# Kernel tuning notes

Hardware: AMD Instinct MI355X
Metric: run time of the kernel (lower is better)

## Reference

```python
import jax, jax.numpy as jnp
import numpy as np

N = 50000      # nodes
E = 1600000    # edges (avg degree 32)
IN = 4         # in_size
H = 64         # hidden size


def _gcn_conv(x, W, b, src, dst, ew, n):
    """PyG GCNConv with edge_weight: add self-loops (weight 1), symmetric
    deg^{-1/2} normalization, gather-transform-scatter aggregation, then bias."""
    xw = x @ W  # [n, out] transform first (PyG lin before propagate)
    loops = jnp.arange(n)
    s = jnp.concatenate([src, loops])
    d = jnp.concatenate([dst, loops])
    w = jnp.concatenate([ew, jnp.ones((n,), ew.dtype)])
    deg = jax.ops.segment_sum(w, d, num_segments=n)
    dinv = jnp.where(deg > 0, jax.lax.rsqrt(deg), 0.0)
    norm = dinv[s] * w * dinv[d]                      # [E+n]
    msg = xw[s] * norm[:, None]                       # [E+n, out]
    out = jax.ops.segment_sum(msg, d, num_segments=n)
    return out + b


def _tower(x, src, dst, ew, W0, b0, W1, b1, W2, b2, Wl, bl):
    # basic_gcn: GCNConv+ReLU, GCNConv+ReLU, GCNConv, then nn.Linear(out,out)
    n = x.shape[0]
    h = jax.nn.relu(_gcn_conv(x, W0, b0, src, dst, ew, n))
    h = jax.nn.relu(_gcn_conv(h, W1, b1, src, dst, ew, n))
    h = _gcn_conv(h, W2, b2, src, dst, ew, n)
    return h @ Wl + bl


def setup_inputs() -> dict:
    key = jax.random.key(0)
    ks = jax.random.split(key, 20)
    x = jax.random.normal(ks[0], (N, IN), dtype=jnp.float32)
    edge_index = jax.random.randint(ks[1], (2, E), 0, N, dtype=jnp.int64)
    edge_weights = jax.random.uniform(ks[2], (E,), dtype=jnp.float32)

    def lin(k, fin, fout):
        return jax.random.normal(k, (fin, fout), dtype=jnp.float32) * (1.0 / np.sqrt(fin))

    inp = {"x": x, "edge_index": edge_index, "edge_weights": edge_weights}
    # optim tower: in_size=4 -> 64 -> 64 -> 1, plus Linear(1,1)
    inp["o_W0"], inp["o_b0"] = lin(ks[3], IN, H), jnp.zeros((H,), jnp.float32)
    inp["o_W1"], inp["o_b1"] = lin(ks[4], H, H), jnp.zeros((H,), jnp.float32)
    inp["o_W2"], inp["o_b2"] = lin(ks[5], H, 1), jnp.zeros((1,), jnp.float32)
    inp["o_Wl"], inp["o_bl"] = lin(ks[6], 1, 1), jnp.zeros((1,), jnp.float32)
    # gamma tower: in_size+1=5 -> 64 -> 64 -> 1, plus Linear(1,1)
    inp["g_W0"], inp["g_b0"] = lin(ks[7], IN + 1, H), jnp.zeros((H,), jnp.float32)
    inp["g_W1"], inp["g_b1"] = lin(ks[8], H, H), jnp.zeros((H,), jnp.float32)
    inp["g_W2"], inp["g_b2"] = lin(ks[9], H, 1), jnp.zeros((1,), jnp.float32)
    inp["g_Wl"], inp["g_bl"] = lin(ks[10], 1, 1), jnp.zeros((1,), jnp.float32)
    return inp


def reference(x, edge_index, edge_weights,
              o_W0, o_b0, o_W1, o_b1, o_W2, o_b2, o_Wl, o_bl,
              g_W0, g_b0, g_W1, g_b1, g_W2, g_b2, g_Wl, g_bl):
    src, dst = edge_index[0], edge_index[1]
    # x_sol = optim tower (constraints=None -> no range scaling)
    x_sol = _tower(x, src, dst, edge_weights,
                   o_W0, o_b0, o_W1, o_b1, o_W2, o_b2, o_Wl, o_bl)  # [N,1]
    # gamma tower on cat(x, x_sol[:, -1:]); constraints=[0,1] -> sigmoid scaling
    xin = jnp.concatenate([x, x_sol[:, -1:]], axis=1)               # [N,5]
    g = _tower(xin, src, dst, edge_weights,
               g_W0, g_b0, g_W1, g_b1, g_W2, g_b2, g_Wl, g_bl)      # [N,1]
    gamma = jax.nn.sigmoid(g)  # scale_to_range(x, [0,1])
    # s == g == 1: gated residual combine
    x_new = x[:, -1:] + gamma * (x_sol - x[:, -1:])
    return (x_new, gamma)
```

## Files before the change

kernel.cpp:

```cpp
#include <hip/hip_runtime.h>
#include <hip/hip_fp16.h>
#include <math.h>

#define NN 50000
#define NE 1600000
#define NBK 196
#define EPB 4096
#define CAP 9216

typedef unsigned int u32;
typedef _Float16 f16x8 __attribute__((ext_vector_type(8)));
typedef float f32x4 __attribute__((ext_vector_type(4)));

static inline int cdiv(int a, int b){ return (a + b - 1) / b; }



__global__ void k_bucket(const int* __restrict__ src, const int* __restrict__ dst,
                         const float* __restrict__ ew, int* __restrict__ bcur,
                         int2* __restrict__ seL, int e){
  __shared__ int h[NBK], base[NBK], curL[NBK];
  int t = threadIdx.x;
  for (int b = t; b < NBK; b += 256){ h[b] = 0; curL[b] = 0; }
  __syncthreads();
  int beg = blockIdx.x*EPB;
  int d[16];
  #pragma unroll
  for (int i = 0; i < 16; ++i){
    int idx = beg + t + i*256;
    d[i] = (idx < e) ? dst[idx] : -1;
    if (d[i] >= 0) atomicAdd(&h[d[i] >> 8], 1);
  }
  __syncthreads();
  for (int b = t; b < NBK; b += 256)
    if (h[b] > 0) base[b] = b*CAP + atomicAdd(&bcur[b], h[b]);
  __syncthreads();
  #pragma unroll
  for (int i = 0; i < 16; ++i){
    int idx = beg + t + i*256;
    if (idx >= e) continue;
    int dd = d[i], b = dd >> 8;
    int pos = base[b] + atomicAdd(&curL[b], 1);
    seL[pos] = make_int2(((dd & 255) << 16) | src[idx], __float_as_int(ew[idx]));
  }
}

__global__ void k_csr_bucket(const int* __restrict__ bcur, const int2* __restrict__ seL,
                             const float* __restrict__ x, int* __restrict__ rowS,
                             int* __restrict__ rowE, u32* __restrict__ packed,
                             float* __restrict__ dinv, float* __restrict__ xd, int n){
  __shared__ int hist[256], sh[256], cur[256];
  __shared__ float wsum[256];
  int b = blockIdx.x, t = threadIdx.x;
  int ebeg = b*CAP, eend = ebeg + bcur[b];
  hist[t] = 0; wsum[t] = 0.f;
  __syncthreads();
  for (int i = ebeg + t; i < eend; i += 256)
    atomicAdd(&hist[seL[i].x >> 16], 1);
  __syncthreads();
  int v = hist[t];
  sh[t] = v; __syncthreads();
  for (int o = 1; o < 256; o <<= 1){
    int u = (t >= o) ? sh[t-o] : 0;
    __syncthreads();
    sh[t] += u;
    __syncthreads();
  }
  int rs = ebeg + sh[t] - v;
  int node = b*256 + t;
  if (node < n){ rowS[node] = rs; rowE[node] = rs + v; }
  cur[t] = rs;
  __syncthreads();
  for (int i = ebeg + t; i < eend; i += 256){
    int2 u = seL[i];
    int d = u.x >> 16;
    int pos = atomicAdd(&cur[d], 1);
    float w = __int_as_float(u.y);
    packed[pos] = (u32)(u.x & 0xFFFF) |
                  ((u32)__half_as_ushort(__float2half(w)) << 16);
    atomicAdd(&wsum[d], w);
  }
  __syncthreads();
  if (node < n){
    float di = rsqrtf(1.f + wsum[t]);
    dinv[node] = di;
    float4 xv = ((const float4*)x)[node];
    ((float4*)xd)[node] = make_float4(xv.x*di, xv.y*di, xv.z*di, xv.w*di);
  }
}


__global__ void k_agg4(const int* __restrict__ rowS, const int* __restrict__ rowE,
                       const u32* __restrict__ packed, const float* __restrict__ xd,
                       const float* __restrict__ dinv, float* __restrict__ y4, int n){
  int i = blockIdx.x*256 + threadIdx.x;
  if (i >= n) return;
  float4 self = ((const float4*)xd)[i];
  float ax = self.x, ay = self.y, az = self.z, aw = self.w;
  int end = rowE[i];
  for (int p = rowS[i]; p < end; ++p){
    u32 v = packed[p];
    float w = __half2float(__ushort_as_half((unsigned short)(v >> 16)));
    float4 xs = ((const float4*)xd)[v & 0xFFFF];
    ax = fmaf(w, xs.x, ax);
    ay = fmaf(w, xs.y, ay);
    az = fmaf(w, xs.z, az);
    aw = fmaf(w, xs.w, aw);
  }
  float di = dinv[i];
  ((float4*)y4)[i] = make_float4(ax*di, ay*di, az*di, aw*di);
}

template<int FIN>
__global__ __attribute__((amdgpu_waves_per_eu(2, 4)))
void k_conv2_mfma(const float* __restrict__ y4, const float* __restrict__ yx,
                  const float* __restrict__ W0, const float* __restrict__ b0,
                  const float* __restrict__ W1, const float* __restrict__ dinv,
                  __half* __restrict__ out, int n){
  int lane = threadIdx.x & 63;
  int m = lane & 15, q = lane >> 4;
  int wid = (blockIdx.x*256 + threadIdx.x) >> 6;
  int nw = gridDim.x * 4;

  auto ldB = [&](int kk, int ct){
    f16x8 r;
    #pragma unroll
    for (int j = 0; j < 8; ++j)
      r[j] = (_Float16)W1[(kk*32 + q*8 + j)*64 + ct*16 + m];
    return r;
  };
  f16x8 b00 = ldB(0,0), b01 = ldB(0,1), b02 = ldB(0,2), b03 = ldB(0,3);
  f16x8 b10 = ldB(1,0), b11 = ldB(1,1), b12 = ldB(1,2), b13 = ldB(1,3);

  float w0c[2][FIN][8];
  float b0c[2][8];
  #pragma unroll
  for (int kk = 0; kk < 2; ++kk){
    #pragma unroll
    for (int j = 0; j < 8; ++j) b0c[kk][j] = b0[kk*32 + q*8 + j];
    #pragma unroll
    for (int c = 0; c < FIN; ++c)
      #pragma unroll
      for (int j = 0; j < 8; ++j)
        w0c[kk][c][j] = W0[c*64 + kk*32 + q*8 + j];
  }

  int ntiles = n >> 4;
  for (int tile = wid; tile < ntiles; tile += nw){
    int base = tile << 4;
    float4 yv = ((const float4*)y4)[base + m];
    float y5 = 0.f;
    if constexpr (FIN == 5) y5 = yx[base + m];
    f16x8 a0, a1;
    #pragma unroll
    for (int j = 0; j < 8; ++j){
      float h0 = b0c[0][j], h1 = b0c[1][j];
      h0 = fmaf(yv.x, w0c[0][0][j], h0);  h1 = fmaf(yv.x, w0c[1][0][j], h1);
      h0 = fmaf(yv.y, w0c[0][1][j], h0);  h1 = fmaf(yv.y, w0c[1][1][j], h1);
      h0 = fmaf(yv.z, w0c[0][2][j], h0);  h1 = fmaf(yv.z, w0c[1][2][j], h1);
      h0 = fmaf(yv.w, w0c[0][3][j], h0);  h1 = fmaf(yv.w, w0c[1][3][j], h1);
      if constexpr (FIN == 5){
        h0 = fmaf(y5, w0c[0][4][j], h0);  h1 = fmaf(y5, w0c[1][4][j], h1);
      }
      a0[j] = (_Float16)fmaxf(h0, 0.f);
      a1[j] = (_Float16)fmaxf(h1, 0.f);
    }
    f32x4 c0 = {0,0,0,0}, c1 = {0,0,0,0}, c2 = {0,0,0,0}, c3 = {0,0,0,0};
    c0 = __builtin_amdgcn_mfma_f32_16x16x32_f16(a0, b00, c0, 0, 0, 0);
    c0 = __builtin_amdgcn_mfma_f32_16x16x32_f16(a1, b10, c0, 0, 0, 0);
    c1 = __builtin_amdgcn_mfma_f32_16x16x32_f16(a0, b01, c1, 0, 0, 0);
    c1 = __builtin_amdgcn_mfma_f32_16x16x32_f16(a1, b11, c1, 0, 0, 0);
    c2 = __builtin_amdgcn_mfma_f32_16x16x32_f16(a0, b02, c2, 0, 0, 0);
    c2 = __builtin_amdgcn_mfma_f32_16x16x32_f16(a1, b12, c2, 0, 0, 0);
    c3 = __builtin_amdgcn_mfma_f32_16x16x32_f16(a0, b03, c3, 0, 0, 0);
    c3 = __builtin_amdgcn_mfma_f32_16x16x32_f16(a1, b13, c3, 0, 0, 0);

    float4 dv = ((const float4*)dinv)[tile*4 + q];
    float dvr[4] = {dv.x, dv.y, dv.z, dv.w};
    auto st = [&](const f32x4& c, int ct){
      int ft = ct*16 + m;
      #pragma unroll
      for (int r = 0; r < 4; ++r)
        out[(size_t)(base + q*4 + r)*64 + ft] = __float2half(c[r]*dvr[r]);
    };
    st(c0, 0); st(c1, 1); st(c2, 2); st(c3, 3);
  }
}

__global__ __attribute__((amdgpu_waves_per_eu(4, 8)))
void k_agg64f(const int* __restrict__ rowS, const int* __restrict__ rowE,
              const u32* __restrict__ packed, const __half* __restrict__ xw,
              const float* __restrict__ dinv, const float* __restrict__ b,
              const float* __restrict__ W2, float* __restrict__ shat, int n){
  int tid = blockIdx.x*256 + threadIdx.x;
  int node = tid >> 6, lane = tid & 63;
  if (node >= n) return;
  int f2 = lane & 31, ep = lane >> 5;
  const __half2* xw2 = (const __half2*)xw;
  float ax = 0.f, ay = 0.f;
  int p = rowS[node], end = rowE[node];

  auto proc = [&](u32 myv, int t){
    u32 v0 = __builtin_amdgcn_readlane(myv, 2*t);
    u32 v1 = __builtin_amdgcn_readlane(myv, 2*t + 1);
    u32 v = ep ? v1 : v0;
    int s = v & 0xFFFF;
    float w = __half2float(__ushort_as_half((unsigned short)(v >> 16)));
    float2 xf = __half22float2(xw2[s*32 + f2]);
    ax = fmaf(w, xf.x, ax);
    ay = fmaf(w, xf.y, ay);
  };

  for (; p + 64 <= end; p += 64){
    u32 myv = __builtin_nontemporal_load(&packed[p + lane]);
    #pragma unroll
    for (int t = 0; t < 32; ++t) proc(myv, t);
  }
  int rem = end - p;
  if (rem > 0){
    u32 myv = (lane < rem) ? packed[p + lane] : 0u;
    #pragma unroll
    for (int t = 0; t < 16; ++t) proc(myv, t);
    if (rem > 32){
      #pragma unroll
      for (int t = 16; t < 32; ++t) proc(myv, t);
    }
  }

  ax += __shfl_xor(ax, 32, 64);
  ay += __shfl_xor(ay, 32, 64);
  float di = dinv[node];
  float2 sf = __half22float2(xw2[(size_t)node*32 + f2]);
  float hx = (ax + sf.x)*di + b[2*f2];
  float hy = (ay + sf.y)*di + b[2*f2 + 1];
  float2 w2 = ((const float2*)W2)[f2];
  float part = fmaxf(hx, 0.f)*w2.x + fmaxf(hy, 0.f)*w2.y;
  part += __shfl_xor(part, 16, 64);
  part += __shfl_xor(part, 8, 64);
  part += __shfl_xor(part, 4, 64);
  part += __shfl_xor(part, 2, 64);
  part += __shfl_xor(part, 1, 64);
  if (lane == 0) shat[node] = part * di;
}


__global__ void k_agg1_xsol(const int* __restrict__ rowS, const int* __restrict__ rowE,
                            const u32* __restrict__ packed, const float* __restrict__ shat,
                            const float* __restrict__ dinv, const float* __restrict__ b,
                            const float* __restrict__ Wl, const float* __restrict__ bl,
                            float* __restrict__ xsol, float* __restrict__ xsolh, int n){
  int tid = blockIdx.x*256 + threadIdx.x;
  int node = tid >> 5, l = tid & 31;
  if (node >= n) return;
  int beg = rowS[node], end = rowE[node];
  float acc = 0.f;
  for (int p = beg + l; p < end; p += 32){
    u32 v = packed[p];
    float w = __half2float(__ushort_as_half((unsigned short)(v >> 16)));
    acc = fmaf(w, shat[v & 0xFFFF], acc);
  }
  acc += __shfl_xor(acc, 16, 64);
  acc += __shfl_xor(acc, 8, 64);
  acc += __shfl_xor(acc, 4, 64);
  acc += __shfl_xor(acc, 2, 64);
  acc += __shfl_xor(acc, 1, 64);
  if (l == 0){
    float di = dinv[node];
    float h = (acc + shat[node])*di + b[0];
    float v = h*Wl[0] + bl[0];
    xsol[node]  = v;
    xsolh[node] = v*di;
  }
}

__global__ void k_agg1s(const int* __restrict__ rowS, const int* __restrict__ rowE,
                        const u32* __restrict__ packed, const float* __restrict__ xsh,
                        const float* __restrict__ dinv, float* __restrict__ yx, int n){
  int tid = blockIdx.x*256 + threadIdx.x;
  int node = tid >> 5, l = tid & 31;
  if (node >= n) return;
  int beg = rowS[node], end = rowE[node];
  float acc = 0.f;
  for (int p = beg + l; p < end; p += 32){
    u32 v = packed[p];
    float w = __half2float(__ushort_as_half((unsigned short)(v >> 16)));
    acc = fmaf(w, xsh[v & 0xFFFF], acc);
  }
  acc += __shfl_xor(acc, 16, 64);
  acc += __shfl_xor(acc, 8, 64);
  acc += __shfl_xor(acc, 4, 64);
  acc += __shfl_xor(acc, 2, 64);
  acc += __shfl_xor(acc, 1, 64);
  if (l == 0)
    yx[node] = (acc + xsh[node]) * dinv[node];
}

__global__ void k_agg1_final(const int* __restrict__ rowS, const int* __restrict__ rowE,
                             const u32* __restrict__ packed, const float* __restrict__ shat,
                             const float* __restrict__ dinv, const float* __restrict__ b,
                             const float* __restrict__ Wl, const float* __restrict__ bl,
                             const float* __restrict__ xsol, const float* __restrict__ x,
                             float* __restrict__ out, int n){
  int tid = blockIdx.x*256 + threadIdx.x;
  int node = tid >> 5, l = tid & 31;
  if (node >= n) return;
  int beg = rowS[node], end = rowE[node];
  float acc = 0.f;
  for (int p = beg + l; p < end; p += 32){
    u32 v = packed[p];
    float w = __half2float(__ushort_as_half((unsigned short)(v >> 16)));
    acc = fmaf(w, shat[v & 0xFFFF], acc);
  }
  acc += __shfl_xor(acc, 16, 64);
  acc += __shfl_xor(acc, 8, 64);
  acc += __shfl_xor(acc, 4, 64);
  acc += __shfl_xor(acc, 2, 64);
  acc += __shfl_xor(acc, 1, 64);
  if (l == 0){
    float di = dinv[node];
    float g = ((acc + shat[node])*di + b[0])*Wl[0] + bl[0];
    float gamma = 1.f / (1.f + expf(-g));
    float xl = x[node*4+3];
    out[node]     = xl + gamma*(xsol[node] - xl);
    out[n + node] = gamma;
  }
}


extern "C" void kernel_launch(void* const* d_in, const int* in_sizes, int n_in,
                              void* d_out, int out_size, void* d_ws, size_t ws_size,
                              hipStream_t stream){
  const float* x   = (const float*)d_in[0];
  const int*   ei  = (const int*)d_in[1];
  const float* ew  = (const float*)d_in[2];
  const float* oW0 = (const float*)d_in[3];
  const float* ob0 = (const float*)d_in[4];
  const float* oW1 = (const float*)d_in[5];
  const float* ob1 = (const float*)d_in[6];
  const float* oW2 = (const float*)d_in[7];
  const float* ob2 = (const float*)d_in[8];
  const float* oWl = (const float*)d_in[9];
  const float* obl = (const float*)d_in[10];
  const float* gW0 = (const float*)d_in[11];
  const float* gb0 = (const float*)d_in[12];
  const float* gW1 = (const float*)d_in[13];
  const float* gb1 = (const float*)d_in[14];
  const float* gW2 = (const float*)d_in[15];
  const float* gb2 = (const float*)d_in[16];
  const float* gWl = (const float*)d_in[17];
  const float* gbl = (const float*)d_in[18];

  const int n = NN, e = NE;
  const int* src = ei;
  const int* dst = ei + e;

  char* wsb = (char*)d_ws;
  int2*  seL    = (int2*)wsb;      wsb += (size_t)NBK*CAP*sizeof(int2);
  u32*   packed = (u32*)wsb;       wsb += (size_t)NBK*CAP*4;
  __half* bufA  = (__half*)wsb;    wsb += (size_t)n*64*2;
  float* y4     = (float*)wsb;     wsb += (size_t)n*4*4;
  float* xd     = (float*)wsb;     wsb += (size_t)n*4*4;
  int*   rowS   = (int*)wsb;       wsb += (size_t)n*4;
  int*   rowE   = (int*)wsb;       wsb += (size_t)n*4;
  int*   bcur   = (int*)wsb;       wsb += 256*4;
  float* dinv   = (float*)wsb;     wsb += (size_t)n*4;
  float* shat   = (float*)wsb;     wsb += (size_t)n*4;
  float* xsol   = (float*)wsb;     wsb += (size_t)n*4;
  float* xsolh  = (float*)wsb;     wsb += (size_t)n*4;
  float* yx     = (float*)wsb;     wsb += (size_t)n*4;

  dim3 b256(256);
  int gn  = cdiv(n, 256);
  int gw  = cdiv(n*64, 256);
  int gw2 = cdiv(n*32, 256);
  int gb  = cdiv(e, EPB);
  int gxm = 512;

  hipMemsetAsync(bcur, 0, 256*4, stream);
  k_bucket    <<<gb,  b256, 0, stream>>>(src, dst, ew, bcur, seL, e);
  k_csr_bucket<<<NBK, b256, 0, stream>>>(bcur, seL, x, rowS, rowE, packed, dinv, xd, n);

  k_agg4      <<<gn,  b256, 0, stream>>>(rowS, rowE, packed, xd, dinv, y4, n);

  k_conv2_mfma<4><<<gxm, b256, 0, stream>>>(y4, nullptr, oW0, ob0, oW1, dinv, bufA, n);
  k_agg64f       <<<gw,  b256, 0, stream>>>(rowS, rowE, packed, bufA, dinv, ob1, oW2, shat, n);
  k_agg1_xsol    <<<gw2, b256, 0, stream>>>(rowS, rowE, packed, shat, dinv, ob2, oWl, obl, xsol, xsolh, n);

  k_agg1s        <<<gw2, b256, 0, stream>>>(rowS, rowE, packed, xsolh, dinv, yx, n);
  k_conv2_mfma<5><<<gxm, b256, 0, stream>>>(y4, yx, gW0, gb0, gW1, dinv, bufA, n);
  k_agg64f       <<<gw,  b256, 0, stream>>>(rowS, rowE, packed, bufA, dinv, gb1, gW2, shat, n);
  k_agg1_final   <<<gw2, b256, 0, stream>>>(rowS, rowE, packed, shat, dinv, gb2, gWl, gbl, xsol, x, (float*)d_out, n);
}
```

Before: 295.0 us.

## Fuse gamma-tower scalar aggregation into conv2 MFMA kernel and stage bucket edges in LDS

Removes the separate k_agg1s launch and instead computes the aggregated fifth input feature inside k_conv2_mfma<5>. Each of the four quads per node lane gathers every fourth edge and the partial sums are combined with shuffles. The CSR bucket kernel now copies each bucket's edges into a 72KB shared buffer on the first pass and accumulates the weight sums there, so the second pass reads LDS rather than global memory. This saves one launch and the yx round trip, but adds irregular gathers inside the MFMA kernel and large LDS use that limits occupancy in the bucket kernel.

```diff
diff --git a/kernel.cpp b/kernel.cpp
--- a/kernel.cpp
+++ b/kernel.cpp
@@ -49,14 +49,21 @@
                              const float* __restrict__ x, int* __restrict__ rowS,
                              int* __restrict__ rowE, u32* __restrict__ packed,
                              float* __restrict__ dinv, float* __restrict__ xd, int n){
+  __shared__ int2 eb[CAP];
   __shared__ int hist[256], sh[256], cur[256];
   __shared__ float wsum[256];
   int b = blockIdx.x, t = threadIdx.x;
-  int ebeg = b*CAP, eend = ebeg + bcur[b];
+  int cnt = bcur[b];
+  int ebeg = b*CAP;
   hist[t] = 0; wsum[t] = 0.f;
   __syncthreads();
-  for (int i = ebeg + t; i < eend; i += 256)
-    atomicAdd(&hist[seL[i].x >> 16], 1);
+  for (int i = t; i < cnt; i += 256){
+    int2 u = seL[ebeg + i];
+    eb[i] = u;
+    int d = u.x >> 16;
+    atomicAdd(&hist[d], 1);
+    atomicAdd(&wsum[d], __int_as_float(u.y));
+  }
   __syncthreads();
   int v = hist[t];
   sh[t] = v; __syncthreads();
@@ -71,14 +78,12 @@
   if (node < n){ rowS[node] = rs; rowE[node] = rs + v; }
   cur[t] = rs;
   __syncthreads();
-  for (int i = ebeg + t; i < eend; i += 256){
-    int2 u = seL[i];
+  for (int i = t; i < cnt; i += 256){
+    int2 u = eb[i];
     int d = u.x >> 16;
     int pos = atomicAdd(&cur[d], 1);
-    float w = __int_as_float(u.y);
     packed[pos] = (u32)(u.x & 0xFFFF) |
-                  ((u32)__half_as_ushort(__float2half(w)) << 16);
-    atomicAdd(&wsum[d], w);
+                  ((u32)__half_as_ushort(__float2half(__int_as_float(u.y))) << 16);
   }
   __syncthreads();
   if (node < n){
@@ -113,7 +118,9 @@
 
 template<int FIN>
 __global__ __attribute__((amdgpu_waves_per_eu(2, 4)))
-void k_conv2_mfma(const float* __restrict__ y4, const float* __restrict__ yx,
+void k_conv2_mfma(const float* __restrict__ y4,
+                  const int* __restrict__ rowS, const int* __restrict__ rowE,
+                  const u32* __restrict__ packed, const float* __restrict__ xsolh,
                   const float* __restrict__ W0, const float* __restrict__ b0,
                   const float* __restrict__ W1, const float* __restrict__ dinv,
                   __half* __restrict__ out, int n){
@@ -150,7 +157,26 @@
     int base = tile << 4;
     float4 yv = ((const float4*)y4)[base + m];
     float y5 = 0.f;
-    if constexpr (FIN == 5) y5 = yx[base + m];
+    if constexpr (FIN == 5){
+      int node = base + m;
+      int p0 = rowS[node] + q, end = rowE[node];
+      float acc = 0.f;
+      auto eproc = [&](int p){
+        u32 v = (p < end) ? packed[p] : 0u;
+        float w = __half2float(__ushort_as_half((unsigned short)(v >> 16)));
+        acc = fmaf(w, xsolh[v & 0xFFFF], acc);
+      };
+      #pragma unroll
+      for (int tt = 0; tt < 8; ++tt) eproc(p0 + 4*tt);
+      if (p0 + 32 < end){
+        #pragma unroll
+        for (int tt = 8; tt < 16; ++tt) eproc(p0 + 4*tt);
+      }
+      for (int p = p0 + 64; p < end; p += 4) eproc(p);
+      acc += __shfl_xor(acc, 16, 64);
+      acc += __shfl_xor(acc, 32, 64);
+      y5 = (acc + xsolh[node]) * dinv[node];
+    }
     f16x8 a0, a1;
     #pragma unroll
     for (int j = 0; j < 8; ++j){
@@ -271,28 +297,6 @@
     xsol[node]  = v;
     xsolh[node] = v*di;
   }
-}
-
-__global__ void k_agg1s(const int* __restrict__ rowS, const int* __restrict__ rowE,
-                        const u32* __restrict__ packed, const float* __restrict__ xsh,
-                        const float* __restrict__ dinv, float* __restrict__ yx, int n){
-  int tid = blockIdx.x*256 + threadIdx.x;
-  int node = tid >> 5, l = tid & 31;
-  if (node >= n) return;
-  int beg = rowS[node], end = rowE[node];
-  float acc = 0.f;
-  for (int p = beg + l; p < end; p += 32){
-    u32 v = packed[p];
-    float w = __half2float(__ushort_as_half((unsigned short)(v >> 16)));
-    acc = fmaf(w, xsh[v & 0xFFFF], acc);
-  }
-  acc += __shfl_xor(acc, 16, 64);
-  acc += __shfl_xor(acc, 8, 64);
-  acc += __shfl_xor(acc, 4, 64);
-  acc += __shfl_xor(acc, 2, 64);
-  acc += __shfl_xor(acc, 1, 64);
-  if (l == 0)
-    yx[node] = (acc + xsh[node]) * dinv[node];
 }
 
 __global__ void k_agg1_final(const int* __restrict__ rowS, const int* __restrict__ rowE,
@@ -367,7 +371,6 @@
   float* shat   = (float*)wsb;     wsb += (size_t)n*4;
   float* xsol   = (float*)wsb;     wsb += (size_t)n*4;
   float* xsolh  = (float*)wsb;     wsb += (size_t)n*4;
-  float* yx     = (float*)wsb;     wsb += (size_t)n*4;
 
   dim3 b256(256);
   int gn  = cdiv(n, 256);
@@ -382,12 +385,13 @@
 
   k_agg4      <<<gn,  b256, 0, stream>>>(rowS, rowE, packed, xd, dinv, y4, n);
 
-  k_conv2_mfma<4><<<gxm, b256, 0, stream>>>(y4, nullptr, oW0, ob0, oW1, dinv, bufA, n);
+  k_conv2_mfma<4><<<gxm, b256, 0, stream>>>(y4, rowS, rowE, packed, nullptr,
+                                            oW0, ob0, oW1, dinv, bufA, n);
   k_agg64f       <<<gw,  b256, 0, stream>>>(rowS, rowE, packed, bufA, dinv, ob1, oW2, shat, n);
   k_agg1_xsol    <<<gw2, b256, 0, stream>>>(rowS, rowE, packed, shat, dinv, ob2, oWl, obl, xsol, xsolh, n);
 
-  k_agg1s        <<<gw2, b256, 0, stream>>>(rowS, rowE, packed, xsolh, dinv, yx, n);
-  k_conv2_mfma<5><<<gxm, b256, 0, stream>>>(y4, yx, gW0, gb0, gW1, dinv, bufA, n);
+  k_conv2_mfma<5><<<gxm, b256, 0, stream>>>(y4, rowS, rowE, packed, xsolh,
+                                            gW0, gb0, gW1, dinv, bufA, n);
   k_agg64f       <<<gw,  b256, 0, stream>>>(rowS, rowE, packed, bufA, dinv, gb1, gW2, shat, n);
   k_agg1_final   <<<gw2, b256, 0, stream>>>(rowS, rowE, packed, shat, dinv, gb2, gWl, gbl, xsol, x, (float*)d_out, n);
 }
```

Result: no change. 293.3 us (-0.6%).
